# Optimization experiments

Measured on AMD Instinct MI355X. Metric: run time of the kernel, lower is better.

Reference implementation:

```python
import jax, jax.numpy as jnp
import numpy as np

D_MODEL = 1024
DK = 64
N_HEADS = D_MODEL // DK
MASK = True


def setup_inputs() -> dict:
    key = jax.random.key(0)
    ks = jax.random.split(key, 8)
    B, S = 4, 2048
    scale = 1.0 / np.sqrt(D_MODEL)
    return {
        "query_data": jax.random.normal(ks[0], (B, S, D_MODEL), dtype=jnp.float32),
        "key_data": jax.random.normal(ks[1], (B, S, D_MODEL), dtype=jnp.float32),
        "value_data": jax.random.normal(ks[2], (B, S, D_MODEL), dtype=jnp.float32),
        "Wq": jax.random.normal(ks[3], (D_MODEL, D_MODEL), dtype=jnp.float32) * scale,
        "Wk": jax.random.normal(ks[4], (D_MODEL, D_MODEL), dtype=jnp.float32) * scale,
        "Wv": jax.random.normal(ks[5], (D_MODEL, D_MODEL), dtype=jnp.float32) * scale,
        "Wp": jax.random.normal(ks[6], (D_MODEL, D_MODEL), dtype=jnp.float32) * scale,
        "bp": jnp.zeros((D_MODEL,), dtype=jnp.float32),
    }


def reference(query_data, key_data, value_data, Wq, Wk, Wv, Wp, bp):
    B, S, _ = query_data.shape
    # QKV projections, split into heads: (B, H, S, dk)
    def split_heads(x, W):
        return (x @ W.T).reshape(B, -1, N_HEADS, DK).transpose(0, 2, 1, 3)

    q = split_heads(query_data, Wq)
    k = split_heads(key_data, Wk)
    v = split_heads(value_data, Wv)

    scores = jnp.einsum("bhqd,bhkd->bhqk", q, k) / np.sqrt(DK).astype(np.float32)
    if MASK:
        Sq, Sk = scores.shape[-2], scores.shape[-1]
        causal = jnp.triu(jnp.ones((Sq, Sk), dtype=scores.dtype), k=1) * jnp.float32(-1e13)
        scores = scores + causal  # broadcast over (B, H)
    attn = jax.nn.softmax(scores, axis=-1)
    out = jnp.einsum("bhqk,bhkd->bhqd", attn, v)
    out = out.transpose(0, 2, 1, 3).reshape(B, S, D_MODEL)
    # dropout is identity in eval mode
    return out @ Wp.T + bp
```

## Files before the change

kernel.cpp:

```cpp
#include <hip/hip_runtime.h>
#include <hip/hip_bf16.h>
#include <stdint.h>

#define D_MODEL 1024
#define SEQ     2048
#define BATCH   4
#define NH      16
#define DKK     64
#define MROWS   (BATCH * SEQ)

typedef unsigned short u16;
using bf16x8 = __attribute__((ext_vector_type(8))) __bf16;
using f32x4  = __attribute__((ext_vector_type(4))) float;

__device__ __forceinline__ u16 f2bf(float f) {
    union { float f; uint32_t u; } v; v.f = f;
    return (u16)((v.u + 0x7FFFu + ((v.u >> 16) & 1u)) >> 16);
}
__device__ __forceinline__ uint32_t pk2bf(float a, float b) {
    union { __hip_bfloat162 h; uint32_t u; } v;
    v.h = __float22bfloat162_rn(float2{a, b});
    return v.u;
}

__device__ __forceinline__ float fast_exp2(float x) {
    float r; asm("v_exp_f32 %0, %1" : "=v"(r) : "v"(x)); return r;
}
__device__ __forceinline__ float fast_rcp(float x) {
    float r; asm("v_rcp_f32 %0, %1" : "=v"(r) : "v"(x)); return r;
}

__device__ __forceinline__ void gl_lds16(const u16* g, u16* l) {
    __builtin_amdgcn_global_load_lds(
        (__attribute__((address_space(1))) void*)(const_cast<u16*>(g)),
        (__attribute__((address_space(3))) void*)l, 16, 0, 0);
}

__global__ __launch_bounds__(256) void cvt3_kernel(const float* __restrict__ a,
                                                   const float* __restrict__ b,
                                                   const float* __restrict__ c,
                                                   u16* __restrict__ da,
                                                   u16* __restrict__ db,
                                                   u16* __restrict__ dc) {
    const int i = blockIdx.x * 256 + threadIdx.x;
    const int sel = i >> 21, off = i & ((1 << 21) - 1);
    const float* s = (sel == 0) ? a : (sel == 1) ? b : c;
    u16* d = (sel == 0) ? da : (sel == 1) ? db : dc;
    float4 v = ((const float4*)s)[off];
    uint2 o;
    o.x = pk2bf(v.x, v.y); o.y = pk2bf(v.z, v.w);
    ((uint2*)d)[off] = o;
}

__global__ __launch_bounds__(256) void cvt4_kernel(const float* __restrict__ a,
                                                   const float* __restrict__ b,
                                                   const float* __restrict__ c,
                                                   const float* __restrict__ d4,
                                                   u16* __restrict__ da,
                                                   u16* __restrict__ db,
                                                   u16* __restrict__ dc,
                                                   u16* __restrict__ dd) {
    const int i = blockIdx.x * 256 + threadIdx.x;
    const int sel = i >> 18, off = i & ((1 << 18) - 1);
    const float* s = (sel == 0) ? a : (sel == 1) ? b : (sel == 2) ? c : d4;
    u16* d = (sel == 0) ? da : (sel == 1) ? db : (sel == 2) ? dc : dd;
    float4 v = ((const float4*)s)[off];
    uint2 o;
    o.x = pk2bf(v.x, v.y); o.y = pk2bf(v.z, v.w);
    ((uint2*)d)[off] = o;
}

__global__ __launch_bounds__(256, 3) void gemm_qkv(const u16* __restrict__ XQ,
                                                   const u16* __restrict__ XK,
                                                   const u16* __restrict__ XV,
                                                   const u16* __restrict__ WQ,
                                                   const u16* __restrict__ WK,
                                                   const u16* __restrict__ WV,
                                                   u16* __restrict__ Qo,
                                                   u16* __restrict__ Ko,
                                                   u16* __restrict__ Vto) {
    constexpr int K = 1024, N = 1024;
    __shared__ __align__(16) u16 smem[17408];
    u16* ldsA = smem;
    u16* ldsB = smem + 8192;
    u16* ldsT = smem;

    const int which = blockIdx.x >> 9;
    const int inner = blockIdx.x & 511;
    const u16* A  = (which == 0) ? XQ : (which == 1) ? XK : XV;
    const u16* Bw = (which == 0) ? WQ : (which == 1) ? WK : WV;

    const int t = threadIdx.x;
    const int w = t >> 6, lane = t & 63;
    const int quad = lane >> 4, l15 = lane & 15;
    const int x = inner & 7, j = inner >> 3;
    const int bm = x * 8 + (j >> 3), bn = j & 7;
    const int wm = (w >> 1) * 64, wn = (w & 1) * 64;

    const u16* Ab = A  + (size_t)bm * 128 * K;
    const u16* Bb = Bw + (size_t)bn * 128 * K;
    const int srow  = lane >> 2;
    const int scol8 = (lane & 3) * 8;

    f32x4 acc[4][4];
    #pragma unroll
    for (int i = 0; i < 4; ++i)
        #pragma unroll
        for (int jj = 0; jj < 4; ++jj)
            acc[i][jj] = f32x4{0.f, 0.f, 0.f, 0.f};

    #pragma unroll
    for (int i = 0; i < 2; ++i) {
        const int c = w * 2 + i;
        gl_lds16(Ab + (size_t)(c * 16 + srow) * K + scol8, &ldsA[c * 512]);
        gl_lds16(Bb + (size_t)(c * 16 + srow) * K + scol8, &ldsB[c * 512]);
    }

    int cur = 0;
    for (int k0 = 0; k0 < K; k0 += 32) {
        __syncthreads();
        if (k0 + 32 < K) {
            const int nxt = cur ^ 1;
            #pragma unroll
            for (int i = 0; i < 2; ++i) {
                const int c = w * 2 + i;
                gl_lds16(Ab + (size_t)(c * 16 + srow) * K + k0 + 32 + scol8, &ldsA[nxt * 4096 + c * 512]);
                gl_lds16(Bb + (size_t)(c * 16 + srow) * K + k0 + 32 + scol8, &ldsB[nxt * 4096 + c * 512]);
            }
        }

        bf16x8 afr[4], bfr[4];
        #pragma unroll
        for (int i = 0; i < 4; ++i)
            afr[i] = *(const bf16x8*)&ldsA[cur * 4096 + (wm + i * 16 + l15) * 32 + quad * 8];
        #pragma unroll
        for (int jj = 0; jj < 4; ++jj)
            bfr[jj] = *(const bf16x8*)&ldsB[cur * 4096 + (wn + jj * 16 + l15) * 32 + quad * 8];

        #pragma unroll
        for (int i = 0; i < 4; ++i)
            #pragma unroll
            for (int jj = 0; jj < 4; ++jj)
                acc[i][jj] = __builtin_amdgcn_mfma_f32_16x16x32_bf16(afr[i], bfr[jj], acc[i][jj], 0, 0, 0);
        cur ^= 1;
    }

    if (which < 2) {
        u16* outb = which ? Ko : Qo;
        #pragma unroll
        for (int i = 0; i < 4; ++i)
            #pragma unroll
            for (int jj = 0; jj < 4; ++jj)
                #pragma unroll
                for (int r = 0; r < 4; ++r) {
                    const int row = bm * 128 + wm + i * 16 + quad * 4 + r;
                    const int col = bn * 128 + wn + jj * 16 + l15;
                    outb[(size_t)row * N + col] = f2bf(acc[i][jj][r]);
                }
    } else {
        __syncthreads();
        #pragma unroll
        for (int i = 0; i < 4; ++i)
            #pragma unroll
            for (int jj = 0; jj < 4; ++jj)
                #pragma unroll
                for (int r = 0; r < 4; ++r) {
                    const int row_l = wm + i * 16 + quad * 4 + r;
                    const int col_l = wn + jj * 16 + l15;
                    ldsT[col_l * 136 + row_l] = f2bf(acc[i][jj][r]);
                }
        __syncthreads();
        const int c = t >> 1, half = t & 1;
        const int colg = bn * 128 + c;
        const int hh = colg >> 6, dd = colg & 63;
        const int bb = bm >> 4;
        const int s0 = ((bm * 128) & 2047) + half * 64;
        const u16* srcl = ldsT + c * 136 + half * 64;
        u16* dstg = Vto + (size_t)((bb * NH + hh) * DKK + dd) * SEQ + s0;
        #pragma unroll
        for (int k = 0; k < 8; ++k)
            *(uint4*)(dstg + k * 8) = *(const uint4*)(srcl + k * 8);
    }
}

__global__ __launch_bounds__(256, 3) void gemm_proj(const u16* __restrict__ A,
                                                    const u16* __restrict__ Bw,
                                                    float* __restrict__ outf,
                                                    const float* __restrict__ bias) {
    constexpr int K = 1024, N = 1024;
    __shared__ __align__(16) u16 ldsA[2 * 4096];
    __shared__ __align__(16) u16 ldsB[2 * 4096];

    const int t = threadIdx.x;
    const int w = t >> 6, lane = t & 63;
    const int quad = lane >> 4, l15 = lane & 15;
    const int x = blockIdx.x & 7, j = blockIdx.x >> 3;
    const int bm = x * 8 + ((j & 63) >> 3), bn = j & 7;
    const int wm = (w >> 1) * 64, wn = (w & 1) * 64;

    const u16* Ab = A  + (size_t)bm * 128 * K;
    const u16* Bb = Bw + (size_t)bn * 128 * K;
    const int srow  = lane >> 2;
    const int scol8 = (lane & 3) * 8;

    f32x4 acc[4][4];
    #pragma unroll
    for (int i = 0; i < 4; ++i)
        #pragma unroll
        for (int jj = 0; jj < 4; ++jj)
            acc[i][jj] = f32x4{0.f, 0.f, 0.f, 0.f};

    #pragma unroll
    for (int i = 0; i < 2; ++i) {
        const int c = w * 2 + i;
        gl_lds16(Ab + (size_t)(c * 16 + srow) * K + scol8, &ldsA[c * 512]);
        gl_lds16(Bb + (size_t)(c * 16 + srow) * K + scol8, &ldsB[c * 512]);
    }

    int cur = 0;
    for (int k0 = 0; k0 < K; k0 += 32) {
        __syncthreads();
        if (k0 + 32 < K) {
            const int nxt = cur ^ 1;
            #pragma unroll
            for (int i = 0; i < 2; ++i) {
                const int c = w * 2 + i;
                gl_lds16(Ab + (size_t)(c * 16 + srow) * K + k0 + 32 + scol8, &ldsA[nxt * 4096 + c * 512]);
                gl_lds16(Bb + (size_t)(c * 16 + srow) * K + k0 + 32 + scol8, &ldsB[nxt * 4096 + c * 512]);
            }
        }

        bf16x8 afr[4], bfr[4];
        #pragma unroll
        for (int i = 0; i < 4; ++i)
            afr[i] = *(const bf16x8*)&ldsA[cur * 4096 + (wm + i * 16 + l15) * 32 + quad * 8];
        #pragma unroll
        for (int jj = 0; jj < 4; ++jj)
            bfr[jj] = *(const bf16x8*)&ldsB[cur * 4096 + (wn + jj * 16 + l15) * 32 + quad * 8];

        #pragma unroll
        for (int i = 0; i < 4; ++i)
            #pragma unroll
            for (int jj = 0; jj < 4; ++jj)
                acc[i][jj] = __builtin_amdgcn_mfma_f32_16x16x32_bf16(afr[i], bfr[jj], acc[i][jj], 0, 0, 0);
        cur ^= 1;
    }

    #pragma unroll
    for (int i = 0; i < 4; ++i)
        #pragma unroll
        for (int jj = 0; jj < 4; ++jj)
            #pragma unroll
            for (int r = 0; r < 4; ++r) {
                const int row = bm * 128 + wm + i * 16 + quad * 4 + r;
                const int col = bn * 128 + wn + jj * 16 + l15;
                outf[(size_t)row * N + col] = acc[i][jj][r] + bias[col];
            }
}

__global__ __launch_bounds__(256, 3) void flash_attn(const u16* __restrict__ Qb,
                                                     const u16* __restrict__ Kb,
                                                     const u16* __restrict__ Vt,
                                                     u16* __restrict__ O) {
    __shared__ __align__(16) u16 ldsK[2 * 4096];
    __shared__ __align__(16) u16 ldsV[2 * 4096];
    __shared__ __align__(16) u16 ldsP[4 * 2048];

    const int t = threadIdx.x;
    const int w = t >> 6, lane = t & 63;
    const int quad = lane >> 4, l15 = lane & 15;
    const int bh = blockIdx.x & 63;
    const int qt = 15 - (blockIdx.x >> 6);
    const int b = bh >> 4, h = bh & 15;
    const int q0 = qt * 128;
    const int qw = q0 + w * 32;

    const int srow  = lane >> 2;
    const int scol8 = (lane & 3) * 8;
    const size_t kbase = (size_t)b * SEQ * D_MODEL + h * DKK;
    const size_t vbase = (size_t)(bh * DKK) * SEQ;

    bf16x8 qf[2][2];
    #pragma unroll
    for (int g = 0; g < 2; ++g) {
        const u16* Qrow = Qb + (size_t)(b * SEQ + qw + g * 16 + l15) * D_MODEL + h * DKK;
        qf[g][0] = *(const bf16x8*)(Qrow + quad * 8);
        qf[g][1] = *(const bf16x8*)(Qrow + 32 + quad * 8);
    }

    f32x4 o_acc[2][4];
    #pragma unroll
    for (int g = 0; g < 2; ++g)
        #pragma unroll
        for (int nt = 0; nt < 4; ++nt) o_acc[g][nt] = f32x4{0.f, 0.f, 0.f, 0.f};
    float m_i[2] = {-1e30f, -1e30f}, l_i[2] = {0.f, 0.f};

    const float C2 = 0.18033688f;
    u16* PwS = &ldsP[w * 2048];

    const int ntiles = 2 * qt + 2;

    #pragma unroll
    for (int i = 0; i < 2; ++i) {
        const int e = w * 2 + i, ch = e >> 2, rb = (e & 3) * 16;
        gl_lds16(Kb + kbase + (size_t)(rb + srow) * D_MODEL + ch * 32 + scol8,
                 &ldsK[ch * 2048 + rb * 32]);
        gl_lds16(Vt + vbase + (size_t)(rb + srow) * SEQ + ch * 32 + scol8,
                 &ldsV[ch * 2048 + rb * 32]);
    }

    int cur = 0;
    for (int it = 0; it < ntiles; ++it) {
        const int kb = it * 64;
        __syncthreads();

        if (it + 1 < ntiles) {
            const int nb = kb + 64, nxt = cur ^ 1;
            #pragma unroll
            for (int i = 0; i < 2; ++i) {
                const int e = w * 2 + i, ch = e >> 2, rb = (e & 3) * 16;
                gl_lds16(Kb + kbase + (size_t)(nb + rb + srow) * D_MODEL + ch * 32 + scol8,
                         &ldsK[nxt * 4096 + ch * 2048 + rb * 32]);
                gl_lds16(Vt + vbase + (size_t)(rb + srow) * SEQ + nb + ch * 32 + scol8,
                         &ldsV[nxt * 4096 + ch * 2048 + rb * 32]);
            }
        }

        if (kb <= qw + 31) {
            f32x4 sc[2][4];
            #pragma unroll
            for (int g = 0; g < 2; ++g)
                #pragma unroll
                for (int jt = 0; jt < 4; ++jt) sc[g][jt] = f32x4{0.f, 0.f, 0.f, 0.f};
            #pragma unroll
            for (int ks = 0; ks < 2; ++ks)
                #pragma unroll
                for (int jt = 0; jt < 4; ++jt) {
                    bf16x8 kf = *(const bf16x8*)&ldsK[cur * 4096 + ks * 2048 + (jt * 16 + l15) * 32 + quad * 8];
                    #pragma unroll
                    for (int g = 0; g < 2; ++g)
                        sc[g][jt] = __builtin_amdgcn_mfma_f32_16x16x32_bf16(kf, qf[g][ks], sc[g][jt], 0, 0, 0);
                }

            if (kb + 63 >= qw) {
                #pragma unroll
                for (int g = 0; g < 2; ++g)
                    #pragma unroll
                    for (int jt = 0; jt < 4; ++jt)
                        #pragma unroll
                        for (int r = 0; r < 4; ++r)
                            if (kb + jt * 16 + quad * 4 + r > qw + g * 16 + l15) sc[g][jt][r] = -3.0e38f;
            }

            float alpha[2];
            #pragma unroll
            for (int g = 0; g < 2; ++g) {
                float tmax = sc[g][0][0];
                #pragma unroll
                for (int jt = 0; jt < 4; ++jt)
                    #pragma unroll
                    for (int r = 0; r < 4; ++r) tmax = fmaxf(tmax, sc[g][jt][r]);
                tmax = fmaxf(tmax, __shfl_xor(tmax, 16));
                tmax = fmaxf(tmax, __shfl_xor(tmax, 32));

                const float mn = fmaxf(m_i[g], tmax * C2);
                alpha[g] = fast_exp2(m_i[g] - mn);
                m_i[g] = mn;

                float tsum = 0.f;
                #pragma unroll
                for (int jt = 0; jt < 4; ++jt) {
                    float p[4];
                    #pragma unroll
                    for (int r = 0; r < 4; ++r) {
                        p[r] = fast_exp2(fmaf(sc[g][jt][r], C2, -mn));
                        tsum += p[r];
                    }
                    const int pos = (4 * jt + quad) ^ l15;
                    uint2 pk;
                    pk.x = pk2bf(p[0], p[1]);
                    pk.y = pk2bf(p[2], p[3]);
                    *(uint2*)&PwS[g * 1024 + l15 * 64 + pos * 4] = pk;
                }
                tsum += __shfl_xor(tsum, 16);
                tsum += __shfl_xor(tsum, 32);
                l_i[g] = fmaf(l_i[g], alpha[g], tsum);
            }

            #pragma unroll
            for (int g = 0; g < 2; ++g) {
                float al[4];
                #pragma unroll
                for (int r = 0; r < 4; ++r)
                    al[r] = __shfl(alpha[g], (lane & 48) | (quad * 4 + r));
                #pragma unroll
                for (int nt = 0; nt < 4; ++nt)
                    #pragma unroll
                    for (int r = 0; r < 4; ++r)
                        o_acc[g][nt][r] *= al[r];
            }

            asm volatile("s_waitcnt lgkmcnt(0)" ::: "memory");

            #pragma unroll
            for (int ks = 0; ks < 2; ++ks) {
                const int gg = 8 * ks + 2 * quad;
                union { bf16x8 v; uint2 u[2]; } pu[2];
                #pragma unroll
                for (int g = 0; g < 2; ++g) {
                    pu[g].u[0] = *(const uint2*)&PwS[g * 1024 + l15 * 64 + ((gg) ^ l15) * 4];
                    pu[g].u[1] = *(const uint2*)&PwS[g * 1024 + l15 * 64 + ((gg + 1) ^ l15) * 4];
                }
                #pragma unroll
                for (int nt = 0; nt < 4; ++nt) {
                    bf16x8 vf = *(const bf16x8*)&ldsV[cur * 4096 + ks * 2048 + (nt * 16 + l15) * 32 + quad * 8];
                    #pragma unroll
                    for (int g = 0; g < 2; ++g)
                        o_acc[g][nt] = __builtin_amdgcn_mfma_f32_16x16x32_bf16(pu[g].v, vf, o_acc[g][nt], 0, 0, 0);
                }
            }
        }

        cur ^= 1;
    }

    #pragma unroll
    for (int g = 0; g < 2; ++g) {
        const float rli = fast_rcp(l_i[g]);
        float rl[4];
        #pragma unroll
        for (int r = 0; r < 4; ++r)
            rl[r] = __shfl(rli, (lane & 48) | (quad * 4 + r));
        #pragma unroll
        for (int nt = 0; nt < 4; ++nt)
            #pragma unroll
            for (int r = 0; r < 4; ++r) {
                const int qg = qw + g * 16 + quad * 4 + r;
                O[(size_t)(b * SEQ + qg) * D_MODEL + h * DKK + nt * 16 + l15] = f2bf(o_acc[g][nt][r] * rl[r]);
            }
    }
}

extern "C" void kernel_launch(void* const* d_in, const int* in_sizes, int n_in,
                              void* d_out, int out_size, void* d_ws, size_t ws_size,
                              hipStream_t stream) {
    const float* q_in = (const float*)d_in[0];
    const float* k_in = (const float*)d_in[1];
    const float* v_in = (const float*)d_in[2];
    const float* Wq   = (const float*)d_in[3];
    const float* Wk   = (const float*)d_in[4];
    const float* Wv   = (const float*)d_in[5];
    const float* Wp   = (const float*)d_in[6];
    const float* bp   = (const float*)d_in[7];
    float* out = (float*)d_out;

    char* ws = (char*)d_ws;
    u16* XQ  = (u16*)(ws + (size_t)0);
    u16* XK  = (u16*)(ws + ((size_t)16 << 20));
    u16* XV  = (u16*)(ws + ((size_t)32 << 20));
    u16* WQb = (u16*)(ws + ((size_t)48 << 20));
    u16* WKb = (u16*)(ws + ((size_t)50 << 20));
    u16* WVb = (u16*)(ws + ((size_t)52 << 20));
    u16* WPb = (u16*)(ws + ((size_t)54 << 20));
    u16* Qb  = (u16*)(ws + ((size_t)56 << 20));
    u16* Kb  = (u16*)(ws + ((size_t)72 << 20));
    u16* Vtb = (u16*)(ws + ((size_t)88 << 20));

    cvt3_kernel<<<3 * (1 << 21) / 256, 256, 0, stream>>>(q_in, k_in, v_in, XQ, XK, XV);
    cvt4_kernel<<<4 * (1 << 18) / 256, 256, 0, stream>>>(Wq, Wk, Wv, Wp, WQb, WKb, WVb, WPb);

    gemm_qkv<<<1536, 256, 0, stream>>>(XQ, XK, XV, WQb, WKb, WVb, Qb, Kb, Vtb);

    flash_attn<<<BATCH * NH * (SEQ / 128), 256, 0, stream>>>(Qb, Kb, Vtb, XQ);

    gemm_proj<<<512, 256, 0, stream>>>(XQ, WPb, out, bp);
}
```

Baseline: 314.2 us.

## Keep P in registers via bpermute, lazily rescale softmax, raise occupancy

Drops the per-wave LDS staging buffer for the softmax probabilities and instead rearranges the packed bf16 P fragments across lanes with ds_bpermute, so they can feed the PV MFMA directly. It also skips the running-max rescale of the output accumulator unless any lane's new max exceeds the old one by more than a threshold. Launch bounds are raised to 4 blocks per CU, using the freed LDS. The aim is to cut LDS traffic and wait stalls and to raise occupancy, at the cost of extra permute instructions, higher register pressure, and a small numerical-range risk from the deferred rescale.

```diff
diff --git a/kernel.cpp b/kernel.cpp
--- a/kernel.cpp
+++ b/kernel.cpp
@@ -258,13 +258,12 @@
             }
 }
 
-__global__ __launch_bounds__(256, 3) void flash_attn(const u16* __restrict__ Qb,
+__global__ __launch_bounds__(256, 4) void flash_attn(const u16* __restrict__ Qb,
                                                      const u16* __restrict__ Kb,
                                                      const u16* __restrict__ Vt,
                                                      u16* __restrict__ O) {
     __shared__ __align__(16) u16 ldsK[2 * 4096];
     __shared__ __align__(16) u16 ldsV[2 * 4096];
-    __shared__ __align__(16) u16 ldsP[4 * 2048];
 
     const int t = threadIdx.x;
     const int w = t >> 6, lane = t & 63;
@@ -275,6 +274,11 @@
     const int q0 = qt * 128;
     const int qw = q0 + w * 32;
 
+    const int s0own = (lane >> 4) & 1;
+    const int srcA  = ((lane & 16) << 1) | ((lane & 32) >> 1) | l15;
+    const int srcB  = srcA ^ 16;
+    const bool hi5  = (lane & 32) != 0;
+
     const int srow  = lane >> 2;
     const int scol8 = (lane & 3) * 8;
     const size_t kbase = (size_t)b * SEQ * D_MODEL + h * DKK;
@@ -296,7 +300,6 @@
     float m_i[2] = {-1e30f, -1e30f}, l_i[2] = {0.f, 0.f};
 
     const float C2 = 0.18033688f;
-    u16* PwS = &ldsP[w * 2048];
 
     const int ntiles = 2 * qt + 2;
 
@@ -352,20 +355,28 @@
                             if (kb + jt * 16 + quad * 4 + r > qw + g * 16 + l15) sc[g][jt][r] = -3.0e38f;
             }
 
-            float alpha[2];
+            uint32_t pw[2][4][2];
+            float alpha[2] = {1.f, 1.f};
+            bool resc[2];
             #pragma unroll
             for (int g = 0; g < 2; ++g) {
-                float tmax = sc[g][0][0];
+                float tm[4];
                 #pragma unroll
                 for (int jt = 0; jt < 4; ++jt)
-                    #pragma unroll
-                    for (int r = 0; r < 4; ++r) tmax = fmaxf(tmax, sc[g][jt][r]);
+                    tm[jt] = fmaxf(fmaxf(sc[g][jt][0], sc[g][jt][1]),
+                                   fmaxf(sc[g][jt][2], sc[g][jt][3]));
+                float tmax = fmaxf(fmaxf(tm[0], tm[1]), fmaxf(tm[2], tm[3]));
                 tmax = fmaxf(tmax, __shfl_xor(tmax, 16));
                 tmax = fmaxf(tmax, __shfl_xor(tmax, 32));
 
-                const float mn = fmaxf(m_i[g], tmax * C2);
-                alpha[g] = fast_exp2(m_i[g] - mn);
-                m_i[g] = mn;
+                const float mx = tmax * C2;
+                resc[g] = !__all(mx <= m_i[g] + 8.0f);
+                if (resc[g]) {
+                    const float mn2 = fmaxf(m_i[g], mx);
+                    alpha[g] = fast_exp2(m_i[g] - mn2);
+                    m_i[g] = mn2;
+                }
+                const float mn = m_i[g];
 
                 float tsum = 0.f;
                 #pragma unroll
@@ -376,47 +387,53 @@
                         p[r] = fast_exp2(fmaf(sc[g][jt][r], C2, -mn));
                         tsum += p[r];
                     }
-                    const int pos = (4 * jt + quad) ^ l15;
-                    uint2 pk;
-                    pk.x = pk2bf(p[0], p[1]);
-                    pk.y = pk2bf(p[2], p[3]);
-                    *(uint2*)&PwS[g * 1024 + l15 * 64 + pos * 4] = pk;
+                    pw[g][jt][0] = pk2bf(p[0], p[1]);
+                    pw[g][jt][1] = pk2bf(p[2], p[3]);
                 }
                 tsum += __shfl_xor(tsum, 16);
                 tsum += __shfl_xor(tsum, 32);
-                l_i[g] = fmaf(l_i[g], alpha[g], tsum);
+                l_i[g] = resc[g] ? fmaf(l_i[g], alpha[g], tsum) : (l_i[g] + tsum);
             }
 
             #pragma unroll
             for (int g = 0; g < 2; ++g) {
-                float al[4];
-                #pragma unroll
-                for (int r = 0; r < 4; ++r)
-                    al[r] = __shfl(alpha[g], (lane & 48) | (quad * 4 + r));
-                #pragma unroll
-                for (int nt = 0; nt < 4; ++nt)
+                if (resc[g]) {
+                    float al[4];
                     #pragma unroll
                     for (int r = 0; r < 4; ++r)
-                        o_acc[g][nt][r] *= al[r];
-            }
-
-            asm volatile("s_waitcnt lgkmcnt(0)" ::: "memory");
+                        al[r] = __shfl(alpha[g], (lane & 48) | (quad * 4 + r));
+                    #pragma unroll
+                    for (int nt = 0; nt < 4; ++nt)
+                        #pragma unroll
+                        for (int r = 0; r < 4; ++r)
+                            o_acc[g][nt][r] *= al[r];
+                }
+            }
 
             #pragma unroll
             for (int ks = 0; ks < 2; ++ks) {
-                const int gg = 8 * ks + 2 * quad;
-                union { bf16x8 v; uint2 u[2]; } pu[2];
+                union { bf16x8 v; uint32_t u[4]; } pa[2];
                 #pragma unroll
                 for (int g = 0; g < 2; ++g) {
-                    pu[g].u[0] = *(const uint2*)&PwS[g * 1024 + l15 * 64 + ((gg) ^ l15) * 4];
-                    pu[g].u[1] = *(const uint2*)&PwS[g * 1024 + l15 * 64 + ((gg + 1) ^ l15) * 4];
+                    uint32_t r1[2], r2[2];
+                    #pragma unroll
+                    for (int i = 0; i < 2; ++i) {
+                        const uint32_t a = pw[g][2 * ks][i];
+                        const uint32_t bb2 = pw[g][2 * ks + 1][i];
+                        r1[i] = (uint32_t)__builtin_amdgcn_ds_bpermute(srcA << 2, (int)(s0own ? bb2 : a));
+                        r2[i] = (uint32_t)__builtin_amdgcn_ds_bpermute(srcB << 2, (int)(s0own ? a : bb2));
+                    }
+                    pa[g].u[0] = hi5 ? r2[0] : r1[0];
+                    pa[g].u[1] = hi5 ? r2[1] : r1[1];
+                    pa[g].u[2] = hi5 ? r1[0] : r2[0];
+                    pa[g].u[3] = hi5 ? r1[1] : r2[1];
                 }
                 #pragma unroll
                 for (int nt = 0; nt < 4; ++nt) {
                     bf16x8 vf = *(const bf16x8*)&ldsV[cur * 4096 + ks * 2048 + (nt * 16 + l15) * 32 + quad * 8];
                     #pragma unroll
                     for (int g = 0; g < 2; ++g)
-                        o_acc[g][nt] = __builtin_amdgcn_mfma_f32_16x16x32_bf16(pu[g].v, vf, o_acc[g][nt], 0, 0, 0);
+                        o_acc[g][nt] = __builtin_amdgcn_mfma_f32_16x16x32_bf16(pa[g].v, vf, o_acc[g][nt], 0, 0, 0);
                 }
             }
         }
```

New measurement: 313.3 us. About the same (-0.3%).
